# Optimization experiments

Hardware: AMD Instinct MI355X
Metric: run time of the kernel (lower is better)

The kernel has to match this reference:

```python
import jax, jax.numpy as jnp
import numpy as np

N_DOMAINS = 4          # number of unique domain labels in d
NUM_PROJ = 50          # hard-coded in DiscriminativeSlicedWasserstein.__init__
P_POW = 2              # hard-coded p=2


def setup_inputs() -> dict:
    key = jax.random.key(0)
    k1, k2, k3 = jax.random.split(key, 3)
    N, IN_DIM, OUT_DIM = 32768, 2048, 512
    z = jax.random.normal(k1, (N, IN_DIM), dtype=jnp.float32)
    W = jax.random.normal(k2, (IN_DIM, OUT_DIM), dtype=jnp.float32) * 0.02
    b = jnp.zeros((OUT_DIM,), dtype=jnp.float32)
    # random projections on the unit sphere (rows normalized), as in rand_projections
    P = jax.random.normal(k3, (NUM_PROJ, OUT_DIM), dtype=jnp.float32)
    P = P / jnp.sqrt(jnp.sum(P * P, axis=1, keepdims=True))
    # sorted, equal-count domain labels -> grouping becomes a static reshape
    d = jnp.repeat(jnp.arange(N_DOMAINS, dtype=jnp.int32), N // N_DOMAINS)
    return {"z": z, "W": W, "b": b, "P": P, "d": d}


def reference(z, W, b, P, d):
    # z = self.D(z): linear discriminator
    h = z @ W + b                                   # [N, out_dim]
    per = h.shape[0] // N_DOMAINS
    groups = h.reshape(N_DOMAINS, per, -1)          # [G, n, out_dim] (d is sorted equal-count)
    # project each group onto the random directions: z.matmul(P.T)
    proj = jnp.einsum('gnd,kd->gnk', groups, P)     # [G, n, num_proj]
    # sort along the sample axis (torch sorts each projection's values)
    srt = jnp.sort(proj, axis=1)                    # [G, n, num_proj]
    # all domain pairs (itertools.combinations); equal group sizes => mean of
    # per-pair means == mean over the stacked pair differences
    ii, jj = np.triu_indices(N_DOMAINS, k=1)
    diff = srt[jj] - srt[ii]                        # [n_pairs, n, num_proj]
    loss = jnp.mean(diff ** P_POW)
    return loss
```

## Files before the change

### kernel.cpp

```cpp
#include <hip/hip_runtime.h>

#define NROWS 32768
#define KDIM  2048
#define DDIM  512
#define NPROJ 50
#define NDOM  4
#define NPER  8192
#define BNPAD 64

typedef __attribute__((ext_vector_type(8))) short short8v;
typedef __attribute__((ext_vector_type(4))) float f32x4;

__device__ inline ushort bf16_rne(float x) {
  union { float f; unsigned u; } v; v.f = x;
  unsigned r = v.u + 0x7FFF + ((v.u >> 16) & 1);
  return (ushort)(r >> 16);
}
__device__ inline float bf16_f32(ushort h) {
  union { unsigned u; float f; } v; v.u = ((unsigned)h) << 16;
  return v.f;
}

__global__ __launch_bounds__(256) void wp_kernel(const float* __restrict__ W,
                                                 const float* __restrict__ b,
                                                 const float* __restrict__ P,
                                                 ushort* __restrict__ Bpk,
                                                 float* __restrict__ bp) {
  int idx = blockIdx.x * 256 + threadIdx.x;
  if (idx >= (KDIM + 1) * BNPAD) return;
  int i = idx >> 6;
  int c = idx & 63;
  float acc = 0.f;
  if (c < NPROJ) {
    const float4* row = (const float4*)((i < KDIM) ? (W + (size_t)i * DDIM) : b);
    const float4* pr  = (const float4*)(P + (size_t)c * DDIM);
#pragma unroll 4
    for (int d = 0; d < DDIM / 4; ++d) {
      float4 w = row[d], p = pr[d];
      acc += w.x * p.x + w.y * p.y + w.z * p.z + w.w * p.w;
    }
  }
  if (i < KDIM) {
    int tg = i >> 5, kb = (i >> 3) & 3, e = i & 7;
    int m = c & 15, cf = c >> 4;
    size_t pos = (((size_t)(tg * 4 + cf) * 64) + kb * 16 + m) * 16 + e;
    ushort h = bf16_rne(acc);
    Bpk[pos]     = h;
    Bpk[pos + 8] = bf16_rne(acc - bf16_f32(h));
  } else {
    bp[c] = acc;
  }
}

__device__ __forceinline__ void split8_trunc(const float4 f0, const float4 f1,
                                             short8v& hi, short8v& lo) {
  const float a[8] = {f0.x, f0.y, f0.z, f0.w, f1.x, f1.y, f1.z, f1.w};
  union { unsigned u[4]; short8v s; } H, L;
#pragma unroll
  for (int p = 0; p < 4; ++p) {
    float a0 = a[2 * p], a1 = a[2 * p + 1];
    unsigned u0 = __float_as_uint(a0), u1 = __float_as_uint(a1);
    H.u[p] = __builtin_amdgcn_perm(u1, u0, 0x07060302);
    float l0 = a0 - __uint_as_float(u0 & 0xFFFF0000u);
    float l1 = a1 - __uint_as_float(u1 & 0xFFFF0000u);
    L.u[p] = __builtin_amdgcn_perm(__float_as_uint(l1), __float_as_uint(l0), 0x07060302);
  }
  hi = H.s; lo = L.s;
}

__device__ __forceinline__ void gload16(const float* g, float* l) {
  __builtin_amdgcn_global_load_lds(
      (const __attribute__((address_space(1))) unsigned int*)(unsigned long long)g,
      (__attribute__((address_space(3))) unsigned int*)(unsigned int)(unsigned long long)l,
      16, 0, 0);
}

__global__ __launch_bounds__(256, 1) void gemm_mfma(const float* __restrict__ z,
                                                    const ushort* __restrict__ Bpk,
                                                    const float* __restrict__ bp,
                                                    float* __restrict__ projT) {
  __shared__ __align__(16) float A_lds[2][128 * 64];

  const int tid  = threadIdx.x;
  const int lane = tid & 63;
  const int wave = tid >> 6;
  const int m    = lane & 15;
  const int kb   = lane >> 4;
  const int row0 = blockIdx.x * 128;

  const float* gsrc[8];
#pragma unroll
  for (int i = 0; i < 8; ++i) {
    const int r = wave * 32 + i * 4 + (lane >> 4);
    gsrc[i] = z + (size_t)(row0 + r) * KDIM + (lane & 15) * 4;
  }

#define STAGE(buf_, t_)                                                   \
  {                                                                       \
    _Pragma("unroll")                                                     \
    for (int i = 0; i < 8; ++i)                                           \
      gload16(gsrc[i] + (t_) * 64, &A_lds[buf_][(wave * 32 + i * 4) * 64]); \
  }

  f32x4 acc[2][4];
#pragma unroll
  for (int rf = 0; rf < 2; ++rf)
#pragma unroll
    for (int cf = 0; cf < 4; ++cf) acc[rf][cf] = (f32x4)0.f;

  STAGE(0, 0);
  __syncthreads();

  for (int t = 0; t < 32; ++t) {
    const int buf = t & 1;
    if (t < 31) STAGE(buf ^ 1, t + 1);

    short8v ah[2][2], al[2][2];
#pragma unroll
    for (int rf = 0; rf < 2; ++rf)
#pragma unroll
      for (int ks = 0; ks < 2; ++ks) {
        const float* base = &A_lds[buf][(wave * 32 + rf * 16 + m) * 64 + ks * 32 + kb * 8];
        float4 f0 = *(const float4*)base;
        float4 f1 = *(const float4*)(base + 4);
        split8_trunc(f0, f1, ah[rf][ks], al[rf][ks]);
      }

#pragma unroll
    for (int ks = 0; ks < 2; ++ks) {
      const int tg = t * 2 + ks;
      const uint4* bb = (const uint4*)Bpk + (size_t)tg * 512 + lane * 2;
#pragma unroll
      for (int cf = 0; cf < 4; ++cf) {
        union { uint4 u; short8v s; } bh, bl;
        bh.u = bb[cf * 128];
        bl.u = bb[cf * 128 + 1];
#pragma unroll
        for (int rf = 0; rf < 2; ++rf) {
          acc[rf][cf] = __builtin_amdgcn_mfma_f32_16x16x32_bf16(ah[rf][ks], bh.s, acc[rf][cf], 0, 0, 0);
          acc[rf][cf] = __builtin_amdgcn_mfma_f32_16x16x32_bf16(al[rf][ks], bh.s, acc[rf][cf], 0, 0, 0);
          acc[rf][cf] = __builtin_amdgcn_mfma_f32_16x16x32_bf16(ah[rf][ks], bl.s, acc[rf][cf], 0, 0, 0);
        }
      }
    }
    __syncthreads();
  }
#undef STAGE

  const int g     = row0 >> 13;
  const int nbase = (row0 & (NPER - 1)) + wave * 32;
#pragma unroll
  for (int rf = 0; rf < 2; ++rf)
#pragma unroll
    for (int cf = 0; cf < 4; ++cf) {
      const int col = cf * 16 + m;
      if (col < NPROJ) {
        const float bj = bp[col];
        float* dst = projT + (size_t)(g * NPROJ + col) * NPER + nbase + rf * 16 + kb * 4;
        dst[0] = acc[rf][cf][0] + bj;
        dst[1] = acc[rf][cf][1] + bj;
        dst[2] = acc[rf][cf][2] + bj;
        dst[3] = acc[rf][cf][3] + bj;
      }
    }
}

#define CE(a, b, asc) { float x_ = v[a], y_ = v[b]; \
  if ((asc) ? (x_ > y_) : (x_ < y_)) { v[a] = y_; v[b] = x_; } }

__device__ inline int swz(int i) { return i ^ (((i >> 5) & 7) << 2); }
#define SPAD 8192

template <int JMAX>
__device__ inline void wave_merge(float v[8], int t, int k) {
  const bool asc = (((t << 3) & k) == 0);
#pragma unroll
  for (int j = JMAX; j >= 8; j >>= 1) {
    const int d = j >> 3;
    const bool keepmin = (asc != ((t & d) != 0));
#pragma unroll
    for (int e = 0; e < 8; ++e) {
      float o = __shfl_xor(v[e], d, 64);
      v[e] = keepmin ? fminf(v[e], o) : fmaxf(v[e], o);
    }
  }
  CE(0, 4, asc); CE(1, 5, asc); CE(2, 6, asc); CE(3, 7, asc);
  CE(0, 2, asc); CE(1, 3, asc); CE(4, 6, asc); CE(5, 7, asc);
  CE(0, 1, asc); CE(2, 3, asc); CE(4, 5, asc); CE(6, 7, asc);
}

__global__ __launch_bounds__(1024) void sort_cols(float* __restrict__ projT) {
  __shared__ __align__(16) float sA[SPAD];
  __shared__ __align__(16) float sB[SPAD];
  float* col = projT + (size_t)blockIdx.x * NPER;
  const int t  = threadIdx.x;
  const int i0 = t << 3;
  float v[8];

  *(float4*)&v[0] = *(const float4*)(col + i0);
  *(float4*)&v[4] = *(const float4*)(col + i0 + 4);

  CE(0, 1, true);  CE(2, 3, false); CE(4, 5, true);  CE(6, 7, false);
  CE(0, 2, true);  CE(1, 3, true);  CE(4, 6, false); CE(5, 7, false);
  CE(0, 1, true);  CE(2, 3, true);  CE(4, 5, false); CE(6, 7, false);
  {
    bool d8 = (t & 1) == 0;
    CE(0, 4, d8); CE(1, 5, d8); CE(2, 6, d8); CE(3, 7, d8);
    CE(0, 2, d8); CE(1, 3, d8); CE(4, 6, d8); CE(5, 7, d8);
    CE(0, 1, d8); CE(2, 3, d8); CE(4, 5, d8); CE(6, 7, d8);
  }

  wave_merge<8>(v, t, 16);
  wave_merge<16>(v, t, 32);
  wave_merge<32>(v, t, 64);
  wave_merge<64>(v, t, 128);
  wave_merge<128>(v, t, 256);
  wave_merge<256>(v, t, 512);

  *(float4*)&sA[swz(i0)]     = *(float4*)&v[0];
  *(float4*)&sA[swz(i0 + 4)] = *(float4*)&v[4];
  __syncthreads();
  int cur = 0;

  for (int k = 1024; k <= NPER; k <<= 1) {
    const bool asc = ((i0 & k) == 0);
    for (int j = k >> 1; j >= 512; j >>= 1) {
      const float* src = cur ? sB : sA;
      float*       dst = cur ? sA : sB;
      const int ip = i0 ^ j;
      float4 a0 = *(const float4*)&src[swz(i0)];
      float4 a1 = *(const float4*)&src[swz(i0 + 4)];
      float4 b0 = *(const float4*)&src[swz(ip)];
      float4 b1 = *(const float4*)&src[swz(ip + 4)];
      const bool keepmin = (asc != ((i0 & j) != 0));
      float4 r0, r1;
      if (keepmin) {
        r0.x = fminf(a0.x, b0.x); r0.y = fminf(a0.y, b0.y); r0.z = fminf(a0.z, b0.z); r0.w = fminf(a0.w, b0.w);
        r1.x = fminf(a1.x, b1.x); r1.y = fminf(a1.y, b1.y); r1.z = fminf(a1.z, b1.z); r1.w = fminf(a1.w, b1.w);
      } else {
        r0.x = fmaxf(a0.x, b0.x); r0.y = fmaxf(a0.y, b0.y); r0.z = fmaxf(a0.z, b0.z); r0.w = fmaxf(a0.w, b0.w);
        r1.x = fmaxf(a1.x, b1.x); r1.y = fmaxf(a1.y, b1.y); r1.z = fmaxf(a1.z, b1.z); r1.w = fmaxf(a1.w, b1.w);
      }
      *(float4*)&dst[swz(i0)]     = r0;
      *(float4*)&dst[swz(i0 + 4)] = r1;
      __syncthreads();
      cur ^= 1;
      *(float4*)&v[0] = r0;
      *(float4*)&v[4] = r1;
    }
    wave_merge<256>(v, t, k);
    if (k != NPER) {
      float* d2 = cur ? sB : sA;
      *(float4*)&d2[swz(i0)]     = *(float4*)&v[0];
      *(float4*)&d2[swz(i0 + 4)] = *(float4*)&v[4];
      __syncthreads();
    }
  }

  *(float4*)(col + i0)     = *(float4*)&v[0];
  *(float4*)(col + i0 + 4) = *(float4*)&v[4];
}

__global__ __launch_bounds__(256) void reduce_k(const float* __restrict__ projT,
                                                float* __restrict__ partial) {
  const int k  = blockIdx.x;
  const int nc = blockIdx.y;
  const int n  = nc * 1024 + threadIdx.x * 4;
  const float4 x0 = *(const float4*)(projT + (size_t)(0 * NPROJ + k) * NPER + n);
  const float4 x1 = *(const float4*)(projT + (size_t)(1 * NPROJ + k) * NPER + n);
  const float4 x2 = *(const float4*)(projT + (size_t)(2 * NPROJ + k) * NPER + n);
  const float4 x3 = *(const float4*)(projT + (size_t)(3 * NPROJ + k) * NPER + n);
  const float a0[4] = {x0.x, x0.y, x0.z, x0.w};
  const float a1[4] = {x1.x, x1.y, x1.z, x1.w};
  const float a2[4] = {x2.x, x2.y, x2.z, x2.w};
  const float a3[4] = {x3.x, x3.y, x3.z, x3.w};
  float local = 0.f;
#pragma unroll
  for (int e = 0; e < 4; ++e) {
    float d01 = a0[e] - a1[e], d02 = a0[e] - a2[e], d03 = a0[e] - a3[e];
    float d12 = a1[e] - a2[e], d13 = a1[e] - a3[e], d23 = a2[e] - a3[e];
    local += d01 * d01 + d02 * d02 + d03 * d03 + d12 * d12 + d13 * d13 + d23 * d23;
  }
#pragma unroll
  for (int o = 32; o > 0; o >>= 1) local += __shfl_down(local, o, 64);
  __shared__ float red[4];
  if ((threadIdx.x & 63) == 0) red[threadIdx.x >> 6] = local;
  __syncthreads();
  if (threadIdx.x == 0) partial[nc * NPROJ + k] = red[0] + red[1] + red[2] + red[3];
}

__global__ __launch_bounds__(512) void final_k(const float* __restrict__ partial,
                                               float* __restrict__ out) {
  const int t = threadIdx.x;
  float v = (t < 8 * NPROJ) ? partial[t] : 0.f;
#pragma unroll
  for (int o = 32; o > 0; o >>= 1) v += __shfl_down(v, o, 64);
  __shared__ float red[8];
  if ((t & 63) == 0) red[t >> 6] = v;
  __syncthreads();
  if (t == 0) {
    float s = 0.f;
#pragma unroll
    for (int w = 0; w < 8; ++w) s += red[w];
    out[0] = s * (1.0f / (6.0f * NPER * NPROJ));
  }
}

extern "C" void kernel_launch(void* const* d_in, const int* in_sizes, int n_in,
                              void* d_out, int out_size, void* d_ws, size_t ws_size,
                              hipStream_t stream) {
  const float* z = (const float*)d_in[0];
  const float* W = (const float*)d_in[1];
  const float* b = (const float*)d_in[2];
  const float* P = (const float*)d_in[3];

  float*  projT   = (float*)d_ws;
  ushort* Bpk     = (ushort*)(projT + (size_t)NDOM * NPROJ * NPER);
  float*  bp      = (float*)(Bpk + (size_t)2 * BNPAD * KDIM);
  float*  partial = bp + BNPAD;

  wp_kernel<<<((KDIM + 1) * BNPAD + 255) / 256, 256, 0, stream>>>(W, b, P, Bpk, bp);
  gemm_mfma<<<NROWS / 128, 256, 0, stream>>>(z, Bpk, bp, projT);
  sort_cols<<<NDOM * NPROJ, 1024, 0, stream>>>(projT);
  reduce_k<<<dim3(NPROJ, 8), 256, 0, stream>>>(projT, partial);
  final_k<<<1, 512, 0, stream>>>(partial, (float*)d_out);
}
```

Baseline: 146.3 us.

## Split GEMM K across two blocks, stage B in LDS, fold partials in sort

The GEMM grid doubles by splitting the K dimension in two. Each block writes a partial projection buffer, and the sort kernel adds the two partials when it loads its column. B tiles are now staged in LDS through async global_load_lds alongside a swizzled, smaller A tile. Barriers use explicit vmcnt waits, and the 1-block-per-CU launch bound is dropped to allow more occupancy. The aim is to fill the CUs (256 blocks before) and hide load latency, at the cost of an extra partial buffer write and read.

```diff
diff --git a/kernel.cpp b/kernel.cpp
--- a/kernel.cpp
+++ b/kernel.cpp
@@ -7,6 +7,7 @@
 #define NDOM  4
 #define NPER  8192
 #define BNPAD 64
+#define PELEM ((size_t)NDOM * NPROJ * NPER)
 
 typedef __attribute__((ext_vector_type(8))) short short8v;
 typedef __attribute__((ext_vector_type(4))) float f32x4;
@@ -43,10 +44,10 @@
   if (i < KDIM) {
     int tg = i >> 5, kb = (i >> 3) & 3, e = i & 7;
     int m = c & 15, cf = c >> 4;
-    size_t pos = (((size_t)(tg * 4 + cf) * 64) + kb * 16 + m) * 16 + e;
+    size_t pos = (size_t)(tg * 4 + cf) * 1024 + (kb * 16 + m) * 8 + e;
     ushort h = bf16_rne(acc);
-    Bpk[pos]     = h;
-    Bpk[pos + 8] = bf16_rne(acc - bf16_f32(h));
+    Bpk[pos]       = h;
+    Bpk[pos + 512] = bf16_rne(acc - bf16_f32(h));
   } else {
     bp[c] = acc;
   }
@@ -75,11 +76,12 @@
       16, 0, 0);
 }
 
-__global__ __launch_bounds__(256, 1) void gemm_mfma(const float* __restrict__ z,
-                                                    const ushort* __restrict__ Bpk,
-                                                    const float* __restrict__ bp,
-                                                    float* __restrict__ projT) {
-  __shared__ __align__(16) float A_lds[2][128 * 64];
+__global__ __launch_bounds__(256) void gemm_mfma(const float* __restrict__ z,
+                                                 const ushort* __restrict__ Bpk,
+                                                 const float* __restrict__ bp,
+                                                 float* __restrict__ part) {
+  __shared__ __align__(16) float A_lds[2][4096];
+  __shared__ __align__(16) float B_lds[2][2048];
 
   const int tid  = threadIdx.x;
   const int lane = tid & 63;
@@ -87,19 +89,34 @@
   const int m    = lane & 15;
   const int kb   = lane >> 4;
   const int row0 = blockIdx.x * 128;
-
-  const float* gsrc[8];
-#pragma unroll
-  for (int i = 0; i < 8; ++i) {
-    const int r = wave * 32 + i * 4 + (lane >> 4);
-    gsrc[i] = z + (size_t)(row0 + r) * KDIM + (lane & 15) * 4;
+  const int ksb  = blockIdx.y;
+  const int k0   = ksb * 1024;
+
+  const float* gsrcA[4];
+  const float* gsrcB[2];
+  const float* Bf = (const float*)Bpk;
+#pragma unroll
+  for (int a = 0; a < 4; ++a) {
+    const int i = wave * 4 + a;
+    const int r = i * 8 + (lane >> 3);
+    const int q = (lane & 7) ^ ((lane >> 3) & 7);
+    gsrcA[a] = z + (size_t)(row0 + r) * KDIM + k0 + q * 4;
+  }
+#pragma unroll
+  for (int b2 = 0; b2 < 2; ++b2) {
+    const int j = wave * 2 + b2;
+    gsrcB[b2] = Bf + (size_t)(k0 >> 5) * 2048 + j * 256 + lane * 4;
   }
 
 #define STAGE(buf_, t_)                                                   \
   {                                                                       \
     _Pragma("unroll")                                                     \
-    for (int i = 0; i < 8; ++i)                                           \
-      gload16(gsrc[i] + (t_) * 64, &A_lds[buf_][(wave * 32 + i * 4) * 64]); \
+    for (int a = 0; a < 4; ++a)                                           \
+      gload16(gsrcA[a] + (t_) * 32, &A_lds[buf_][(wave * 4 + a) * 256]);  \
+    _Pragma("unroll")                                                     \
+    for (int b2 = 0; b2 < 2; ++b2)                                        \
+      gload16(gsrcB[b2] + (size_t)(t_) * 2048,                            \
+              &B_lds[buf_][(wave * 2 + b2) * 256]);                       \
   }
 
   f32x4 acc[2][4];
@@ -109,60 +126,73 @@
     for (int cf = 0; cf < 4; ++cf) acc[rf][cf] = (f32x4)0.f;
 
   STAGE(0, 0);
-  __syncthreads();
-
+
+#pragma unroll 2
   for (int t = 0; t < 32; ++t) {
     const int buf = t & 1;
-    if (t < 31) STAGE(buf ^ 1, t + 1);
-
-    short8v ah[2][2], al[2][2];
+
+    if (t < 31) {
+      STAGE(buf ^ 1, t + 1);
+      asm volatile("s_waitcnt vmcnt(6)" ::: "memory");
+    } else {
+      asm volatile("s_waitcnt vmcnt(0)" ::: "memory");
+    }
+    __builtin_amdgcn_s_barrier();
+    __builtin_amdgcn_sched_barrier(0);
+
+    float4 f[2][2];
+#pragma unroll
+    for (int rf = 0; rf < 2; ++rf) {
+      const int r = wave * 32 + rf * 16 + m;
+      const float* base = &A_lds[buf][r * 32];
+      f[rf][0] = *(const float4*)(base + (((kb * 2)     ^ (m & 7)) * 4));
+      f[rf][1] = *(const float4*)(base + (((kb * 2 + 1) ^ (m & 7)) * 4));
+    }
+    short8v bh[4], bl[4];
+    const ushort* Bu = (const ushort*)&B_lds[buf][0];
+#pragma unroll
+    for (int cf = 0; cf < 4; ++cf) {
+      const ushort* fb = Bu + cf * 1024 + lane * 8;
+      bh[cf] = *(const short8v*)fb;
+      bl[cf] = *(const short8v*)(fb + 512);
+    }
+
+    short8v ah[2], al[2];
 #pragma unroll
     for (int rf = 0; rf < 2; ++rf)
-#pragma unroll
-      for (int ks = 0; ks < 2; ++ks) {
-        const float* base = &A_lds[buf][(wave * 32 + rf * 16 + m) * 64 + ks * 32 + kb * 8];
-        float4 f0 = *(const float4*)base;
-        float4 f1 = *(const float4*)(base + 4);
-        split8_trunc(f0, f1, ah[rf][ks], al[rf][ks]);
+      split8_trunc(f[rf][0], f[rf][1], ah[rf], al[rf]);
+
+#pragma unroll
+    for (int cf = 0; cf < 4; ++cf)
+#pragma unroll
+      for (int rf = 0; rf < 2; ++rf) {
+        acc[rf][cf] = __builtin_amdgcn_mfma_f32_16x16x32_bf16(ah[rf], bh[cf], acc[rf][cf], 0, 0, 0);
+        acc[rf][cf] = __builtin_amdgcn_mfma_f32_16x16x32_bf16(al[rf], bh[cf], acc[rf][cf], 0, 0, 0);
+        acc[rf][cf] = __builtin_amdgcn_mfma_f32_16x16x32_bf16(ah[rf], bl[cf], acc[rf][cf], 0, 0, 0);
       }
 
-#pragma unroll
-    for (int ks = 0; ks < 2; ++ks) {
-      const int tg = t * 2 + ks;
-      const uint4* bb = (const uint4*)Bpk + (size_t)tg * 512 + lane * 2;
-#pragma unroll
-      for (int cf = 0; cf < 4; ++cf) {
-        union { uint4 u; short8v s; } bh, bl;
-        bh.u = bb[cf * 128];
-        bl.u = bb[cf * 128 + 1];
-#pragma unroll
-        for (int rf = 0; rf < 2; ++rf) {
-          acc[rf][cf] = __builtin_amdgcn_mfma_f32_16x16x32_bf16(ah[rf][ks], bh.s, acc[rf][cf], 0, 0, 0);
-          acc[rf][cf] = __builtin_amdgcn_mfma_f32_16x16x32_bf16(al[rf][ks], bh.s, acc[rf][cf], 0, 0, 0);
-          acc[rf][cf] = __builtin_amdgcn_mfma_f32_16x16x32_bf16(ah[rf][ks], bl.s, acc[rf][cf], 0, 0, 0);
-        }
-      }
-    }
-    __syncthreads();
+    __builtin_amdgcn_s_barrier();
   }
 #undef STAGE
 
-  const int g     = row0 >> 13;
-  const int nbase = (row0 & (NPER - 1)) + wave * 32;
-#pragma unroll
-  for (int rf = 0; rf < 2; ++rf)
+  const int g = row0 >> 13;
+#pragma unroll
+  for (int rf = 0; rf < 2; ++rf) {
+    const int nbase = (row0 & (NPER - 1)) + wave * 32 + rf * 16 + kb * 4;
 #pragma unroll
     for (int cf = 0; cf < 4; ++cf) {
       const int col = cf * 16 + m;
       if (col < NPROJ) {
-        const float bj = bp[col];
-        float* dst = projT + (size_t)(g * NPROJ + col) * NPER + nbase + rf * 16 + kb * 4;
+        const float bj = (ksb == 0) ? bp[col] : 0.f;
+        float* dst = part + (size_t)ksb * PELEM +
+                     (size_t)(g * NPROJ + col) * NPER + nbase;
         dst[0] = acc[rf][cf][0] + bj;
         dst[1] = acc[rf][cf][1] + bj;
         dst[2] = acc[rf][cf][2] + bj;
         dst[3] = acc[rf][cf][3] + bj;
       }
     }
+  }
 }
 
 #define CE(a, b, asc) { float x_ = v[a], y_ = v[b]; \
@@ -189,16 +219,23 @@
   CE(0, 1, asc); CE(2, 3, asc); CE(4, 5, asc); CE(6, 7, asc);
 }
 
-__global__ __launch_bounds__(1024) void sort_cols(float* __restrict__ projT) {
+__global__ __launch_bounds__(1024) void sort_cols(float* __restrict__ p0,
+                                                  const float* __restrict__ p1) {
   __shared__ __align__(16) float sA[SPAD];
   __shared__ __align__(16) float sB[SPAD];
-  float* col = projT + (size_t)blockIdx.x * NPER;
+  float* col = p0 + (size_t)blockIdx.x * NPER;
   const int t  = threadIdx.x;
   const int i0 = t << 3;
   float v[8];
 
   *(float4*)&v[0] = *(const float4*)(col + i0);
   *(float4*)&v[4] = *(const float4*)(col + i0 + 4);
+  {
+    const float* c1 = p1 + (size_t)blockIdx.x * NPER;
+    float4 a0 = *(const float4*)(c1 + i0), a1 = *(const float4*)(c1 + i0 + 4);
+    v[0] += a0.x; v[1] += a0.y; v[2] += a0.z; v[3] += a0.w;
+    v[4] += a1.x; v[5] += a1.y; v[6] += a1.z; v[7] += a1.w;
+  }
 
   CE(0, 1, true);  CE(2, 3, false); CE(4, 5, true);  CE(6, 7, false);
   CE(0, 2, true);  CE(1, 3, true);  CE(4, 6, false); CE(5, 7, false);
@@ -314,14 +351,15 @@
   const float* b = (const float*)d_in[2];
   const float* P = (const float*)d_in[3];
 
-  float*  projT   = (float*)d_ws;
-  ushort* Bpk     = (ushort*)(projT + (size_t)NDOM * NPROJ * NPER);
+  float*  part0   = (float*)d_ws;
+  float*  part1   = part0 + PELEM;
+  ushort* Bpk     = (ushort*)(part1 + PELEM);
   float*  bp      = (float*)(Bpk + (size_t)2 * BNPAD * KDIM);
   float*  partial = bp + BNPAD;
 
   wp_kernel<<<((KDIM + 1) * BNPAD + 255) / 256, 256, 0, stream>>>(W, b, P, Bpk, bp);
-  gemm_mfma<<<NROWS / 128, 256, 0, stream>>>(z, Bpk, bp, projT);
-  sort_cols<<<NDOM * NPROJ, 1024, 0, stream>>>(projT);
-  reduce_k<<<dim3(NPROJ, 8), 256, 0, stream>>>(projT, partial);
+  gemm_mfma<<<dim3(NROWS / 128, 2), 256, 0, stream>>>(z, Bpk, bp, part0);
+  sort_cols<<<NDOM * NPROJ, 1024, 0, stream>>>(part0, part1);
+  reduce_k<<<dim3(NPROJ, 8), 256, 0, stream>>>(part0, partial);
   final_k<<<1, 512, 0, stream>>>(partial, (float*)d_out);
 }
```

After: 129.4 us. 11.6% less time.
